# Performance work log

Measured on AMD Instinct MI355X. Metric: run time of the kernel, lower is better.

Reference implementation:

```python
import jax, jax.numpy as jnp
import numpy as np

D_MODEL = 1024
N_HEADS = 16
D_K = D_MODEL // N_HEADS
THETA = 10000.0
BATCH, SEQ = 2, 2048


def setup_inputs() -> dict:
    key = jax.random.key(0)
    k1, k2, k3 = jax.random.split(key, 3)
    std_qkv = float(np.sqrt(2.0 / (3 * D_MODEL + D_MODEL)))
    std_o = float(np.sqrt(2.0 / (D_MODEL + D_MODEL)))
    return {
        "x": jax.random.normal(k1, (BATCH, SEQ, D_MODEL), dtype=jnp.float32),
        "w_qkv": jax.random.normal(k2, (3 * D_MODEL, D_MODEL), dtype=jnp.float32) * std_qkv,
        "w_o": jax.random.normal(k3, (D_MODEL, D_MODEL), dtype=jnp.float32) * std_o,
        "token_positions": jnp.arange(SEQ, dtype=jnp.int32),
    }


def _rope(x, token_positions):
    # x: [..., s, d_k]; interleaved rotary embedding
    d_k = x.shape[-1]
    freqs = jnp.arange(0, d_k, 2, dtype=jnp.float32) / d_k          # [d_k/2]
    inv_freqs = 1.0 / (THETA ** freqs)
    angles = token_positions.astype(jnp.float32)[:, None] * inv_freqs  # [s, d_k/2]
    cos, sin = jnp.cos(angles), jnp.sin(angles)
    x_even, x_odd = x[..., 0::2], x[..., 1::2]
    rot_even = x_even * cos - x_odd * sin
    rot_odd = x_even * sin + x_odd * cos
    # interleave back: out[..., 2i] = rot_even[i], out[..., 2i+1] = rot_odd[i]
    return jnp.stack([rot_even, rot_odd], axis=-1).reshape(x.shape)


def reference(x, w_qkv, w_o, token_positions):
    b, s, _ = x.shape
    qkv = jnp.einsum('oi,bsi->bso', w_qkv, x)                        # [b, s, 3*d_model]
    q, k, v = jnp.split(qkv, 3, axis=-1)
    def to_heads(t):
        return t.reshape(b, s, N_HEADS, D_K).transpose(0, 2, 1, 3)  # [b, h, s, d]
    q, k, v = to_heads(q), to_heads(k), to_heads(v)
    q = _rope(q, token_positions)
    k = _rope(k, token_positions)
    scores = jnp.einsum('bhqd,bhkd->bhqk', q, k) / jnp.sqrt(jnp.float32(D_K))
    causal = jnp.tril(jnp.ones((s, s), dtype=bool))
    scores = jnp.where(causal, scores, -jnp.inf)
    attn = jax.nn.softmax(scores, axis=-1)
    y = jnp.einsum('bhqk,bhkd->bhqd', attn, v)
    y = y.transpose(0, 2, 1, 3).reshape(b, s, D_MODEL)
    return jnp.einsum('oi,bsi->bso', w_o, y)
```

## Files before the change

### kernel.cpp

```cpp
#include <hip/hip_runtime.h>
#include <math.h>

#define DEV __device__ __forceinline__

typedef __attribute__((ext_vector_type(8))) short bf16x8;
typedef __attribute__((ext_vector_type(4))) float f32x4;
typedef __attribute__((ext_vector_type(4))) unsigned int u32x4;

typedef __attribute__((address_space(3))) unsigned int lds_u32;
typedef const __attribute__((address_space(1))) unsigned int glb_u32;

DEV void gload16(const unsigned short* g, unsigned short* l) {
  __builtin_amdgcn_global_load_lds((glb_u32*)g, (lds_u32*)l, 16, 0, 0);
}

DEV bf16x8 lds_read8(const unsigned short* base, unsigned int byteoff) {
  return *reinterpret_cast<const bf16x8*>(
      reinterpret_cast<const char*>(base) + byteoff);
}

DEV float fexp2(float x) { return __builtin_amdgcn_exp2f(x); }

DEV unsigned short f2bf(float f) {
  union { float f; unsigned int u; } v; v.f = f;
  unsigned int u = v.u;
  unsigned int r = (u + 0x7fffu + ((u >> 16) & 1u)) >> 16;
  return (unsigned short)r;
}
DEV float bf2f(unsigned short h) {
  union { unsigned int u; float f; } v; v.u = ((unsigned int)h) << 16;
  return v.f;
}
DEV unsigned int cvtpk_bf16(float lo, float hi) {
  unsigned int r;
  asm("v_cvt_pk_bf16_f32 %0, %1, %2" : "=v"(r) : "v"(lo), "v"(hi));
  return r;
}

__global__ void cvt_f32_bf16(const float* __restrict__ in,
                             unsigned short* __restrict__ out, int n4) {
  int stride = gridDim.x * blockDim.x;
  for (int i = blockIdx.x * blockDim.x + threadIdx.x; i < n4; i += stride) {
    float4 f = reinterpret_cast<const float4*>(in)[i];
    ushort4 o;
    o.x = f2bf(f.x); o.y = f2bf(f.y); o.z = f2bf(f.z); o.w = f2bf(f.w);
    reinterpret_cast<ushort4*>(out)[i] = o;
  }
}

template <bool BF16_OUT>
__global__ __launch_bounds__(256) void gemm_bt(const unsigned short* __restrict__ A,
                                               const unsigned short* __restrict__ B,
                                               void* __restrict__ Cv,
                                               int M, int N, int K) {
  __shared__ unsigned short Ab[2][4096];
  __shared__ unsigned short Bb[2][4096];
  const int tid = threadIdx.x;
  const int lane = tid & 63, wid = tid >> 6;
  const int wm = (wid >> 1) * 64, wn = (wid & 1) * 64;
  const int fr = lane & 15, kq = lane >> 4;
  const int arow0 = blockIdx.x * 128;
  const int brow0 = blockIdx.y * 128;

  const int srow = wid * 16 + (lane >> 2), sslot = (lane & 3) * 8;
  const unsigned short* aptr = A + (size_t)(arow0 + srow) * K + sslot;
  const unsigned short* bptr = B + (size_t)(brow0 + srow) * K + sslot;

  unsigned int offa[4], offb[4];
#pragma unroll
  for (int i = 0; i < 4; i++) {
    offa[i] = (unsigned)((wm + i * 16 + fr) * 64 + kq * 16);
    offb[i] = (unsigned)((wn + i * 16 + fr) * 64 + kq * 16);
  }

  f32x4 acc[4][4] = {};
  const int nk = K >> 5;

#define GSTAGE(BI)                                             \
  {                                                            \
    gload16(aptr, &Ab[BI][wid * 512]);                         \
    gload16(aptr + (size_t)64 * K, &Ab[BI][2048 + wid * 512]); \
    gload16(bptr, &Bb[BI][wid * 512]);                         \
    gload16(bptr + (size_t)64 * K, &Bb[BI][2048 + wid * 512]); \
    aptr += 32;                                                \
    bptr += 32;                                                \
  }

#define GCOMP(BI)                                                                     \
  {                                                                                   \
    bf16x8 af[4], bfr[4];                                                             \
    _Pragma("unroll") for (int i = 0; i < 4; i++) af[i] = lds_read8(Ab[BI], offa[i]); \
    _Pragma("unroll") for (int j = 0; j < 4; j++) bfr[j] = lds_read8(Bb[BI], offb[j]); \
    _Pragma("unroll") for (int i = 0; i < 4; i++)                                     \
      _Pragma("unroll") for (int j = 0; j < 4; j++)                                   \
        acc[i][j] = __builtin_amdgcn_mfma_f32_16x16x32_bf16(af[i], bfr[j], acc[i][j], 0, 0, 0); \
  }

  GSTAGE(0);
  for (int ks = 0; ks < nk; ks += 2) {
    __syncthreads();
    GSTAGE(1);
    GCOMP(0);
    __syncthreads();
    if (ks + 2 < nk) GSTAGE(0);
    GCOMP(1);
  }
#undef GSTAGE
#undef GCOMP

#pragma unroll
  for (int i = 0; i < 4; i++) {
#pragma unroll
    for (int j = 0; j < 4; j++) {
#pragma unroll
      for (int r = 0; r < 4; r++) {
        size_t row = (size_t)(arow0 + wm + i * 16 + kq * 4 + r);
        size_t col = (size_t)(brow0 + wn + j * 16 + fr);
        if (BF16_OUT)
          ((unsigned short*)Cv)[row * N + col] = f2bf(acc[i][j][r]);
        else
          ((float*)Cv)[row * N + col] = acc[i][j][r];
      }
    }
  }
}

__global__ __launch_bounds__(256) void rope_kernel(unsigned short* __restrict__ qkv,
                                                   const int* __restrict__ pos) {
  int m = blockIdx.x;
  int s = m & 2047;
  int t = threadIdx.x;
  __shared__ float Cl[32], Sl[32];
  if (t < 32) {
    float position = (float)pos[s];
    float inv = __expf(-(float)t * (9.210340371976184f / 32.0f));
    float ang = position * inv;
    Cl[t] = cosf(ang);
    Sl[t] = sinf(ang);
  }
  __syncthreads();
  const float QS = 0.18033688011112042f;
  int h = t >> 4, g = t & 15;
  float c0 = Cl[2 * g], s0 = Sl[2 * g], c1 = Cl[2 * g + 1], s1 = Sl[2 * g + 1];
  size_t base = (size_t)m * 3072 + h * 64 + 4 * g;
  ushort4 qv = *reinterpret_cast<ushort4*>(&qkv[base]);
  float qe0 = bf2f(qv.x), qo0 = bf2f(qv.y), qe1 = bf2f(qv.z), qo1 = bf2f(qv.w);
  qv.x = f2bf((qe0 * c0 - qo0 * s0) * QS);
  qv.y = f2bf((qe0 * s0 + qo0 * c0) * QS);
  qv.z = f2bf((qe1 * c1 - qo1 * s1) * QS);
  qv.w = f2bf((qe1 * s1 + qo1 * c1) * QS);
  *reinterpret_cast<ushort4*>(&qkv[base]) = qv;
  size_t kb = base + 1024;
  ushort4 kv = *reinterpret_cast<ushort4*>(&qkv[kb]);
  float ke0 = bf2f(kv.x), ko0 = bf2f(kv.y), ke1 = bf2f(kv.z), ko1 = bf2f(kv.w);
  kv.x = f2bf(ke0 * c0 - ko0 * s0);
  kv.y = f2bf(ke0 * s0 + ko0 * c0);
  kv.z = f2bf(ke1 * c1 - ko1 * s1);
  kv.w = f2bf(ke1 * s1 + ko1 * c1);
  *reinterpret_cast<ushort4*>(&qkv[kb]) = kv;
}

__global__ __launch_bounds__(256) void vtrans_kernel(const unsigned short* __restrict__ qkv,
                                                     unsigned short* __restrict__ vt) {
  int bid = blockIdx.x;
  int sb = bid & 31;
  int bh = bid >> 5;
  int h = bh & 15, b = bh >> 4;
  __shared__ unsigned short tile[64][72];
  int t = threadIdx.x;
  int sl = t >> 2, c0 = (t & 3) * 16;
  const unsigned short* src = qkv + (size_t)(b * 2048 + sb * 64) * 3072 + 2048 + h * 64;
  *reinterpret_cast<bf16x8*>(&tile[sl][c0]) =
      *reinterpret_cast<const bf16x8*>(&src[(size_t)sl * 3072 + c0]);
  *reinterpret_cast<bf16x8*>(&tile[sl][c0 + 8]) =
      *reinterpret_cast<const bf16x8*>(&src[(size_t)sl * 3072 + c0 + 8]);
  __syncthreads();
  int d = t >> 2, p0 = (t & 3) * 16;
  unsigned short* dst = vt + ((size_t)bh * 64 + d) * 2048 + sb * 64 + p0;
  bf16x8 o0, o1;
#pragma unroll
  for (int i = 0; i < 8; i++) {
    int p = p0 + i;
    int s_in = (p & 32) + ((p >> 2) & 1) * 16 + ((p >> 3) & 3) * 4 + (p & 3);
    o0[i] = (short)tile[s_in][d];
  }
#pragma unroll
  for (int i = 0; i < 8; i++) {
    int p = p0 + 8 + i;
    int s_in = (p & 32) + ((p >> 2) & 1) * 16 + ((p >> 3) & 3) * 4 + (p & 3);
    o1[i] = (short)tile[s_in][d];
  }
  *reinterpret_cast<bf16x8*>(dst) = o0;
  *reinterpret_cast<bf16x8*>(dst + 8) = o1;
}

__global__ __launch_bounds__(256, 4) void attn_kernel(const unsigned short* __restrict__ qkv,
                                                      const unsigned short* __restrict__ vt,
                                                      unsigned short* __restrict__ Y) {
  int bid = blockIdx.x;
  int bh = bid & 31;
  int qt = 31 - (bid >> 5);
  int h = bh & 15, b = bh >> 4;
  int tid = threadIdx.x, lane = tid & 63, wid = tid >> 6;
  int fr = lane & 15, kq = lane >> 4;
  int qbase = qt * 64 + wid * 16;

  const size_t mrow0 = (size_t)b * 2048;
  const unsigned short* Qp = qkv + (mrow0 + qbase) * 3072 + h * 64;
  const unsigned short* Kp = qkv + mrow0 * 3072 + 1024 + h * 64;
  const unsigned short* Vp = vt + ((size_t)bh * 64) * 2048;

  __shared__ unsigned short Klds[2][4096];
  __shared__ unsigned short Vlds[2][4096];

  bf16x8 qf[2];
#pragma unroll
  for (int ks = 0; ks < 2; ks++)
    qf[ks] = *reinterpret_cast<const bf16x8*>(&Qp[(size_t)fr * 3072 + ks * 32 + kq * 8]);

  const int srow = tid >> 3;
  const int schunk = (tid & 7) ^ (srow & 7);
  const unsigned short* kstage = Kp + (size_t)srow * 3072 + schunk * 8;
  const unsigned short* vstage = Vp + (size_t)srow * 2048 + schunk * 8;

  unsigned int offk[8], offv[8];
#pragma unroll
  for (int g = 0; g < 4; g++)
#pragma unroll
    for (int ks = 0; ks < 2; ks++) {
      int R = g * 16 + fr;
      offk[g * 2 + ks] = (unsigned)(R * 128 + (((4 * ks + kq) ^ (R & 7)) * 16));
    }
#pragma unroll
  for (int db = 0; db < 4; db++)
#pragma unroll
    for (int hf = 0; hf < 2; hf++) {
      int d = db * 16 + fr;
      offv[db * 2 + hf] = (unsigned)(d * 128 + (((4 * hf + kq) ^ (d & 7)) * 16));
    }

  f32x4 acc[4] = {};
  float mr = -1e30f, lr = 0.0f;
  const int q_lane = qbase + fr;
  const int ntiles = qt + 1;

#define STAGE(BI)                                                     \
  {                                                                   \
    gload16(kstage, &Klds[BI][wid * 512]);                            \
    gload16(kstage + (size_t)32 * 3072, &Klds[BI][2048 + wid * 512]); \
    gload16(vstage, &Vlds[BI][wid * 512]);                            \
    gload16(vstage + 32 * 2048, &Vlds[BI][2048 + wid * 512]);         \
    kstage += (size_t)64 * 3072;                                      \
    vstage += 64;                                                     \
  }

#define TILE_COMPUTE(T, BI)                                                           \
  {                                                                                   \
    const int t_ = (T);                                                               \
    const bool masked_ = (t_ == qt);                                                  \
    f32x4 sc[4] = {};                                                                 \
    __builtin_amdgcn_s_setprio(1);                                                    \
    _Pragma("unroll") for (int g = 0; g < 4; g++) {                                   \
      _Pragma("unroll") for (int ks = 0; ks < 2; ks++) {                              \
        bf16x8 kf = lds_read8(Klds[BI], offk[g * 2 + ks]);                            \
        sc[g] = __builtin_amdgcn_mfma_f32_16x16x32_bf16(kf, qf[ks], sc[g], 0, 0, 0);  \
      }                                                                               \
    }                                                                                 \
    __builtin_amdgcn_s_setprio(0);                                                    \
    float s[16];                                                                      \
    _Pragma("unroll") for (int g = 0; g < 4; g++)                                     \
      _Pragma("unroll") for (int r = 0; r < 4; r++) {                                 \
        float v = sc[g][r];                                                           \
        if (masked_) {                                                                \
          int k = t_ * 64 + g * 16 + kq * 4 + r;                                      \
          if (k > q_lane) v = -1e30f;                                                 \
        }                                                                             \
        s[g * 4 + r] = v;                                                             \
      }                                                                               \
                                                        \
    float t0 = fmaxf(fmaxf(s[0], s[1]), s[2]);                                        \
    float t1 = fmaxf(fmaxf(s[3], s[4]), s[5]);                                        \
    float t2 = fmaxf(fmaxf(s[6], s[7]), s[8]);                                        \
    float t3 = fmaxf(fmaxf(s[9], s[10]), s[11]);                                      \
    float t4 = fmaxf(fmaxf(s[12], s[13]), s[14]);                                     \
    float u0 = fmaxf(fmaxf(t0, t1), t2);                                              \
    float u1 = fmaxf(fmaxf(t3, t4), s[15]);                                           \
    float rm = fmaxf(u0, u1);                                                         \
    if (!__all(rm <= mr + 8.0f)) {                                                    \
      float rmf = fmaxf(rm, __shfl_xor(rm, 16));                                      \
      rmf = fmaxf(rmf, __shfl_xor(rmf, 32));                                          \
      float mn = fmaxf(mr, rmf);                                                      \
      float scl = fexp2(mr - mn);                                                     \
      mr = mn;                                                                        \
      lr *= scl;                                                                      \
      _Pragma("unroll") for (int db = 0; db < 4; db++)                                \
        _Pragma("unroll") for (int r = 0; r < 4; r++) acc[db][r] *= scl;              \
    }                                                                                 \
    _Pragma("unroll") for (int i = 0; i < 16; i++) s[i] = fexp2(s[i] - mr);           \
    float a8[8];                                                                      \
    _Pragma("unroll") for (int i = 0; i < 8; i++) a8[i] = s[2 * i] + s[2 * i + 1];    \
    lr += ((a8[0] + a8[1]) + (a8[2] + a8[3])) + ((a8[4] + a8[5]) + (a8[6] + a8[7]));  \
    u32x4 W0 = {cvtpk_bf16(s[0], s[1]), cvtpk_bf16(s[2], s[3]),                       \
                cvtpk_bf16(s[4], s[5]), cvtpk_bf16(s[6], s[7])};                      \
    u32x4 W1 = {cvtpk_bf16(s[8], s[9]), cvtpk_bf16(s[10], s[11]),                     \
                cvtpk_bf16(s[12], s[13]), cvtpk_bf16(s[14], s[15])};                  \
    bf16x8 pa0 = *reinterpret_cast<bf16x8*>(&W0);                                     \
    bf16x8 pa1 = *reinterpret_cast<bf16x8*>(&W1);                                     \
    __builtin_amdgcn_s_setprio(1);                                                    \
    _Pragma("unroll") for (int db = 0; db < 4; db++) {                                \
      bf16x8 vf0 = lds_read8(Vlds[BI], offv[db * 2]);                                 \
      acc[db] = __builtin_amdgcn_mfma_f32_16x16x32_bf16(vf0, pa0, acc[db], 0, 0, 0);  \
      bf16x8 vf1 = lds_read8(Vlds[BI], offv[db * 2 + 1]);                             \
      acc[db] = __builtin_amdgcn_mfma_f32_16x16x32_bf16(vf1, pa1, acc[db], 0, 0, 0);  \
    }                                                                                 \
    __builtin_amdgcn_s_setprio(0);                                                    \
  }

  STAGE(0);
  for (int t = 0; t < ntiles; t += 2) {
    __syncthreads();
    if (t + 1 < ntiles) STAGE(1);
    TILE_COMPUTE(t, 0);
    if (t + 1 >= ntiles) break;
    __syncthreads();
    if (t + 2 < ntiles) STAGE(0);
    TILE_COMPUTE(t + 1, 1);
  }
#undef TILE_COMPUTE
#undef STAGE

  lr += __shfl_xor(lr, 16);
  lr += __shfl_xor(lr, 32);
  float inv = 1.0f / lr;
  unsigned short* yp = Y + (mrow0 + qbase + fr) * 1024 + h * 64 + kq * 4;
#pragma unroll
  for (int db = 0; db < 4; db++) {
    ushort4 o;
    o.x = f2bf(acc[db][0] * inv);
    o.y = f2bf(acc[db][1] * inv);
    o.z = f2bf(acc[db][2] * inv);
    o.w = f2bf(acc[db][3] * inv);
    *reinterpret_cast<ushort4*>(yp + db * 16) = o;
  }
}

extern "C" void kernel_launch(void* const* d_in, const int* in_sizes, int n_in,
                              void* d_out, int out_size, void* d_ws, size_t ws_size,
                              hipStream_t stream) {
  const float* x     = (const float*)d_in[0];
  const float* w_qkv = (const float*)d_in[1];
  const float* w_o   = (const float*)d_in[2];
  const int*   pos   = (const int*)d_in[3];
  float* out = (float*)d_out;

  unsigned char* ws = (unsigned char*)d_ws;
  unsigned short* x_bf    = (unsigned short*)(ws);
  unsigned short* wqkv_bf = (unsigned short*)(ws + 8388608);
  unsigned short* wo_bf   = (unsigned short*)(ws + 14680064);
  unsigned short* qkv     = (unsigned short*)(ws + 16777216);
  unsigned short* vt      = (unsigned short*)(ws + 41943040);
  unsigned short* y       = (unsigned short*)(ws + 50331648);

  cvt_f32_bf16<<<1024, 256, 0, stream>>>(x, x_bf, 4096 * 1024 / 4);
  cvt_f32_bf16<<<1024, 256, 0, stream>>>(w_qkv, wqkv_bf, 3072 * 1024 / 4);
  cvt_f32_bf16<<<512, 256, 0, stream>>>(w_o, wo_bf, 1024 * 1024 / 4);

  gemm_bt<true><<<dim3(32, 24), 256, 0, stream>>>(x_bf, wqkv_bf, (void*)qkv, 4096, 3072, 1024);

  rope_kernel<<<4096, 256, 0, stream>>>(qkv, pos);
  vtrans_kernel<<<1024, 256, 0, stream>>>(qkv, vt);

  attn_kernel<<<1024, 256, 0, stream>>>(qkv, vt, y);

  gemm_bt<false><<<dim3(32, 8), 256, 0, stream>>>(y, wo_bf, (void*)out, 4096, 1024, 1024);
}
```

Measured before the change: 122.5 us.

## Fuse V transpose into QKV GEMM epilogue, swizzle LDS, merge weight conversions

The QKV GEMM now writes the V third of its output directly into the permuted transposed vt layout, which removes the separate vtrans kernel and its extra read and write of V. The two weight conversion launches are merged into one kernel. The GEMM LDS layout gets an XOR swizzle on the k-slot to reduce bank conflicts in the fragment reads. The swizzle and the permuted epilogue indexing must match the attention kernel's expectations exactly, and the vt stores are scattered 8-byte writes.

```diff
diff --git a/kernel.cpp b/kernel.cpp
--- a/kernel.cpp
+++ b/kernel.cpp
@@ -48,66 +48,90 @@
   }
 }
 
+__global__ void cvt2_f32_bf16(const float* __restrict__ ina,
+                              unsigned short* __restrict__ outa, int n4a,
+                              const float* __restrict__ inb,
+                              unsigned short* __restrict__ outb, int n4b) {
+  int stride = gridDim.x * blockDim.x;
+  int total = n4a + n4b;
+  for (int i = blockIdx.x * blockDim.x + threadIdx.x; i < total; i += stride) {
+    if (i < n4a) {
+      float4 f = reinterpret_cast<const float4*>(ina)[i];
+      ushort4 o;
+      o.x = f2bf(f.x); o.y = f2bf(f.y); o.z = f2bf(f.z); o.w = f2bf(f.w);
+      reinterpret_cast<ushort4*>(outa)[i] = o;
+    } else {
+      int j = i - n4a;
+      float4 f = reinterpret_cast<const float4*>(inb)[j];
+      ushort4 o;
+      o.x = f2bf(f.x); o.y = f2bf(f.y); o.z = f2bf(f.z); o.w = f2bf(f.w);
+      reinterpret_cast<ushort4*>(outb)[j] = o;
+    }
+  }
+}
+
+
+#define GEMM_PROLOGUE(A_, B_, K_)                                              \
+  __shared__ unsigned short Ab[2][4096];                                       \
+  __shared__ unsigned short Bb[2][4096];                                       \
+  const int tid = threadIdx.x;                                                 \
+  const int lane = tid & 63, wid = tid >> 6;                                   \
+  const int wm = (wid >> 1) * 64, wn = (wid & 1) * 64;                         \
+  const int fr = lane & 15, kq = lane >> 4;                                    \
+  const int arow0 = blockIdx.x * 128;                                          \
+  const int brow0 = blockIdx.y * 128;                                          \
+  const int srow = wid * 16 + (lane >> 2);                                     \
+  const int sslot = (((lane & 3) ^ ((lane >> 2) & 3))) * 8;                    \
+  const unsigned short* aptr = (A_) + (size_t)(arow0 + srow) * (K_) + sslot;   \
+  const unsigned short* bptr = (B_) + (size_t)(brow0 + srow) * (K_) + sslot;   \
+  unsigned int offa[4], offb[4];                                               \
+  _Pragma("unroll") for (int i = 0; i < 4; i++) {                              \
+    offa[i] = (unsigned)((wm + i * 16 + fr) * 64 + ((kq ^ (fr & 3)) * 16));    \
+    offb[i] = (unsigned)((wn + i * 16 + fr) * 64 + ((kq ^ (fr & 3)) * 16));    \
+  }                                                                            \
+  f32x4 acc[4][4] = {};
+
+#define GSTAGE(BI, K_)                                             \
+  {                                                                \
+    gload16(aptr, &Ab[BI][wid * 512]);                             \
+    gload16(aptr + (size_t)64 * (K_), &Ab[BI][2048 + wid * 512]);  \
+    gload16(bptr, &Bb[BI][wid * 512]);                             \
+    gload16(bptr + (size_t)64 * (K_), &Bb[BI][2048 + wid * 512]);  \
+    aptr += 32;                                                    \
+    bptr += 32;                                                    \
+  }
+
+#define GCOMP(BI)                                                                      \
+  {                                                                                    \
+    bf16x8 af[4], bfr[4];                                                              \
+    _Pragma("unroll") for (int i = 0; i < 4; i++) af[i] = lds_read8(Ab[BI], offa[i]);  \
+    _Pragma("unroll") for (int j = 0; j < 4; j++) bfr[j] = lds_read8(Bb[BI], offb[j]); \
+    _Pragma("unroll") for (int i = 0; i < 4; i++)                                      \
+      _Pragma("unroll") for (int j = 0; j < 4; j++)                                    \
+        acc[i][j] = __builtin_amdgcn_mfma_f32_16x16x32_bf16(af[i], bfr[j], acc[i][j], 0, 0, 0); \
+  }
+
+#define GEMM_MAIN(K_)                       \
+  {                                         \
+    const int nk = (K_) >> 5;     \
+    GSTAGE(0, K_);                          \
+    for (int ks = 0; ks < nk; ks += 2) {    \
+      __syncthreads();                      \
+      GSTAGE(1, K_);                        \
+      GCOMP(0);                             \
+      __syncthreads();                      \
+      if (ks + 2 < nk) GSTAGE(0, K_);       \
+      GCOMP(1);                             \
+    }                                       \
+  }
+
 template <bool BF16_OUT>
 __global__ __launch_bounds__(256) void gemm_bt(const unsigned short* __restrict__ A,
                                                const unsigned short* __restrict__ B,
                                                void* __restrict__ Cv,
                                                int M, int N, int K) {
-  __shared__ unsigned short Ab[2][4096];
-  __shared__ unsigned short Bb[2][4096];
-  const int tid = threadIdx.x;
-  const int lane = tid & 63, wid = tid >> 6;
-  const int wm = (wid >> 1) * 64, wn = (wid & 1) * 64;
-  const int fr = lane & 15, kq = lane >> 4;
-  const int arow0 = blockIdx.x * 128;
-  const int brow0 = blockIdx.y * 128;
-
-  const int srow = wid * 16 + (lane >> 2), sslot = (lane & 3) * 8;
-  const unsigned short* aptr = A + (size_t)(arow0 + srow) * K + sslot;
-  const unsigned short* bptr = B + (size_t)(brow0 + srow) * K + sslot;
-
-  unsigned int offa[4], offb[4];
-#pragma unroll
-  for (int i = 0; i < 4; i++) {
-    offa[i] = (unsigned)((wm + i * 16 + fr) * 64 + kq * 16);
-    offb[i] = (unsigned)((wn + i * 16 + fr) * 64 + kq * 16);
-  }
-
-  f32x4 acc[4][4] = {};
-  const int nk = K >> 5;
-
-#define GSTAGE(BI)                                             \
-  {                                                            \
-    gload16(aptr, &Ab[BI][wid * 512]);                         \
-    gload16(aptr + (size_t)64 * K, &Ab[BI][2048 + wid * 512]); \
-    gload16(bptr, &Bb[BI][wid * 512]);                         \
-    gload16(bptr + (size_t)64 * K, &Bb[BI][2048 + wid * 512]); \
-    aptr += 32;                                                \
-    bptr += 32;                                                \
-  }
-
-#define GCOMP(BI)                                                                     \
-  {                                                                                   \
-    bf16x8 af[4], bfr[4];                                                             \
-    _Pragma("unroll") for (int i = 0; i < 4; i++) af[i] = lds_read8(Ab[BI], offa[i]); \
-    _Pragma("unroll") for (int j = 0; j < 4; j++) bfr[j] = lds_read8(Bb[BI], offb[j]); \
-    _Pragma("unroll") for (int i = 0; i < 4; i++)                                     \
-      _Pragma("unroll") for (int j = 0; j < 4; j++)                                   \
-        acc[i][j] = __builtin_amdgcn_mfma_f32_16x16x32_bf16(af[i], bfr[j], acc[i][j], 0, 0, 0); \
-  }
-
-  GSTAGE(0);
-  for (int ks = 0; ks < nk; ks += 2) {
-    __syncthreads();
-    GSTAGE(1);
-    GCOMP(0);
-    __syncthreads();
-    if (ks + 2 < nk) GSTAGE(0);
-    GCOMP(1);
-  }
-#undef GSTAGE
-#undef GCOMP
-
+  GEMM_PROLOGUE(A, B, K)
+  GEMM_MAIN(K)
 #pragma unroll
   for (int i = 0; i < 4; i++) {
 #pragma unroll
@@ -120,6 +144,50 @@
           ((unsigned short*)Cv)[row * N + col] = f2bf(acc[i][j][r]);
         else
           ((float*)Cv)[row * N + col] = acc[i][j][r];
+      }
+    }
+  }
+}
+
+__global__ __launch_bounds__(256) void gemm_qkv(const unsigned short* __restrict__ A,
+                                                const unsigned short* __restrict__ B,
+                                                unsigned short* __restrict__ qkv,
+                                                unsigned short* __restrict__ vt,
+                                                int K) {
+  const int N = 3072;
+  GEMM_PROLOGUE(A, B, K)
+  GEMM_MAIN(K)
+  if (brow0 < 2048) {
+#pragma unroll
+    for (int i = 0; i < 4; i++) {
+#pragma unroll
+      for (int j = 0; j < 4; j++) {
+#pragma unroll
+        for (int r = 0; r < 4; r++) {
+          size_t row = (size_t)(arow0 + wm + i * 16 + kq * 4 + r);
+          size_t col = (size_t)(brow0 + wn + j * 16 + fr);
+          qkv[row * N + col] = f2bf(acc[i][j][r]);
+        }
+      }
+    }
+  } else {
+#pragma unroll
+    for (int i = 0; i < 4; i++) {
+      int row_base = arow0 + wm + i * 16 + kq * 4;
+      int b = row_base >> 11;
+      int s = row_base & 2047;
+      int p_base = (s & ~31) + 8 * ((s >> 2) & 3) + 4 * ((s >> 4) & 1);
+#pragma unroll
+      for (int j = 0; j < 4; j++) {
+        int col = (brow0 - 2048) + wn + j * 16 + fr;
+        int bh = b * 16 + (col >> 6);
+        int d = col & 63;
+        ushort4 o;
+        o.x = f2bf(acc[i][j][0]);
+        o.y = f2bf(acc[i][j][1]);
+        o.z = f2bf(acc[i][j][2]);
+        o.w = f2bf(acc[i][j][3]);
+        *reinterpret_cast<ushort4*>(&vt[((size_t)bh * 64 + d) * 2048 + p_base]) = o;
       }
     }
   }
@@ -158,40 +226,6 @@
   kv.z = f2bf(ke1 * c1 - ko1 * s1);
   kv.w = f2bf(ke1 * s1 + ko1 * c1);
   *reinterpret_cast<ushort4*>(&qkv[kb]) = kv;
-}
-
-__global__ __launch_bounds__(256) void vtrans_kernel(const unsigned short* __restrict__ qkv,
-                                                     unsigned short* __restrict__ vt) {
-  int bid = blockIdx.x;
-  int sb = bid & 31;
-  int bh = bid >> 5;
-  int h = bh & 15, b = bh >> 4;
-  __shared__ unsigned short tile[64][72];
-  int t = threadIdx.x;
-  int sl = t >> 2, c0 = (t & 3) * 16;
-  const unsigned short* src = qkv + (size_t)(b * 2048 + sb * 64) * 3072 + 2048 + h * 64;
-  *reinterpret_cast<bf16x8*>(&tile[sl][c0]) =
-      *reinterpret_cast<const bf16x8*>(&src[(size_t)sl * 3072 + c0]);
-  *reinterpret_cast<bf16x8*>(&tile[sl][c0 + 8]) =
-      *reinterpret_cast<const bf16x8*>(&src[(size_t)sl * 3072 + c0 + 8]);
-  __syncthreads();
-  int d = t >> 2, p0 = (t & 3) * 16;
-  unsigned short* dst = vt + ((size_t)bh * 64 + d) * 2048 + sb * 64 + p0;
-  bf16x8 o0, o1;
-#pragma unroll
-  for (int i = 0; i < 8; i++) {
-    int p = p0 + i;
-    int s_in = (p & 32) + ((p >> 2) & 1) * 16 + ((p >> 3) & 3) * 4 + (p & 3);
-    o0[i] = (short)tile[s_in][d];
-  }
-#pragma unroll
-  for (int i = 0; i < 8; i++) {
-    int p = p0 + 8 + i;
-    int s_in = (p & 32) + ((p >> 2) & 1) * 16 + ((p >> 3) & 3) * 4 + (p & 3);
-    o1[i] = (short)tile[s_in][d];
-  }
-  *reinterpret_cast<bf16x8*>(dst) = o0;
-  *reinterpret_cast<bf16x8*>(dst + 8) = o1;
 }
 
 __global__ __launch_bounds__(256, 4) void attn_kernel(const unsigned short* __restrict__ qkv,
@@ -277,7 +311,6 @@
         }                                                                             \
         s[g * 4 + r] = v;                                                             \
       }                                                                               \
-                                                        \
     float t0 = fmaxf(fmaxf(s[0], s[1]), s[2]);                                        \
     float t1 = fmaxf(fmaxf(s[3], s[4]), s[5]);                                        \
     float t2 = fmaxf(fmaxf(s[6], s[7]), s[8]);                                        \
@@ -362,13 +395,12 @@
   unsigned short* y       = (unsigned short*)(ws + 50331648);
 
   cvt_f32_bf16<<<1024, 256, 0, stream>>>(x, x_bf, 4096 * 1024 / 4);
-  cvt_f32_bf16<<<1024, 256, 0, stream>>>(w_qkv, wqkv_bf, 3072 * 1024 / 4);
-  cvt_f32_bf16<<<512, 256, 0, stream>>>(w_o, wo_bf, 1024 * 1024 / 4);
-
-  gemm_bt<true><<<dim3(32, 24), 256, 0, stream>>>(x_bf, wqkv_bf, (void*)qkv, 4096, 3072, 1024);
+  cvt2_f32_bf16<<<1024, 256, 0, stream>>>(w_qkv, wqkv_bf, 3072 * 1024 / 4,
+                                          w_o, wo_bf, 1024 * 1024 / 4);
+
+  gemm_qkv<<<dim3(32, 24), 256, 0, stream>>>(x_bf, wqkv_bf, qkv, vt, 1024);
 
   rope_kernel<<<4096, 256, 0, stream>>>(qkv, pos);
-  vtrans_kernel<<<1024, 256, 0, stream>>>(qkv, vt);
 
   attn_kernel<<<1024, 256, 0, stream>>>(qkv, vt, y);
 
```

Result: slower. 126.5 us (+3.3%).
